# Kernel optimization log

Measured on AMD Instinct MI355X. Metric: run time of the kernel, lower is better.

The kernel has to match this reference:

```python
import jax, jax.numpy as jnp
import numpy as np

N = 100000   # nodes
E = 1600000  # edges
D = 64       # in_features == out_features (residual requires equality)
BN_EPS = 1e-5


def setup_inputs() -> dict:
    key = jax.random.key(0)
    ks = jax.random.split(key, 12)
    s = 1.0 / np.sqrt(D)
    inp = {
        "x": jax.random.normal(ks[0], (N, D), dtype=jnp.float32),
        "edge_index": jax.random.randint(ks[1], (2, E), 0, N, dtype=jnp.int64),
        # ResGatedGraphConv params: key/query/value/skip linears
        "Wk": jax.random.uniform(ks[2], (D, D), jnp.float32, -s, s),
        "bk": jax.random.uniform(ks[3], (D,), jnp.float32, -s, s),
        "Wq": jax.random.uniform(ks[4], (D, D), jnp.float32, -s, s),
        "bq": jax.random.uniform(ks[5], (D,), jnp.float32, -s, s),
        "Wv": jax.random.uniform(ks[6], (D, D), jnp.float32, -s, s),
        "bv": jax.random.uniform(ks[7], (D,), jnp.float32, -s, s),
        "Ws": jax.random.uniform(ks[8], (D, D), jnp.float32, -s, s),
        "bs": jax.random.uniform(ks[9], (D,), jnp.float32, -s, s),
        # BatchNorm1d affine params
        "gamma": jnp.ones((D,), jnp.float32),
        "beta": jnp.zeros((D,), jnp.float32),
    }
    return inp


def reference(x, edge_index, Wk, bk, Wq, bq, Wv, bv, Ws, bs, gamma, beta):
    # PyG ResGatedGraphConv:
    #   out_i = W_s x_i + b_s + sum_{(j->i)} sigmoid(k_i + q_j) * v_j
    # where k = lin_key(x), q = lin_query(x), v = lin_value(x).
    src = edge_index[0]  # source nodes j
    dst = edge_index[1]  # target nodes i

    k = x @ Wk.T + bk  # [N, D]
    q = x @ Wq.T + bq  # [N, D]
    v = x @ Wv.T + bv  # [N, D]

    gate = jax.nn.sigmoid(k[dst] + q[src])        # [E, D]
    msg = gate * v[src]                            # [E, D]
    agg = jax.ops.segment_sum(msg, dst, num_segments=x.shape[0])  # [N, D]

    h = agg + x @ Ws.T + bs

    # BatchNorm1d (training mode: batch statistics, biased variance)
    mean = jnp.mean(h, axis=0)
    var = jnp.var(h, axis=0)
    h = (h - mean) * jax.lax.rsqrt(var + BN_EPS) * gamma + beta

    h = jax.nn.relu(h)
    h = h + x  # residual
    # dropout: identity in eval / deterministic reference
    return h
```

## Files before the change

### kernel.cpp

```cpp
#include <hip/hip_runtime.h>
#include <hip/hip_bf16.h>
#include <math.h>

#define N_NODES 100000
#define N_EDGES 1600000
#define D_FEAT  64
#define BN_EPS  1e-5f

#define NBUCKET_PAD 256
#define BUCKET_SHIFT 9
#define NBLK_E  196
#define EPB     8192
#define HIST_TOTAL (NBUCKET_PAD * NBLK_E)
#define NCHUNK_H 98
#define DCAP    14336

typedef __attribute__((ext_vector_type(8))) short bf16x8;
typedef __attribute__((ext_vector_type(4))) float f32x4;

static __device__ __forceinline__ short f2bf(float f) {
    __hip_bfloat16 h = __float2bfloat16(f);
    return __builtin_bit_cast(short, h);
}


__global__ __launch_bounds__(256) void gemm4_mfma_kernel(
    const float* __restrict__ x,
    const float* __restrict__ Wk, const float* __restrict__ bk,
    const float* __restrict__ Wq, const float* __restrict__ bq,
    const float* __restrict__ Wv, const float* __restrict__ bv,
    const float* __restrict__ Ws, const float* __restrict__ bs,
    unsigned short* __restrict__ qvp,
    unsigned short* __restrict__ kp,
    float* __restrict__ h0)
{
    __shared__ short xs[64 * 64];

    const int lane = threadIdx.x & 63;
    const int wave = threadIdx.x >> 6;
    const int r0 = blockIdx.x * 64;

    const float* W; const float* b;
    if      (wave == 0) { W = Wk; b = bk; }
    else if (wave == 1) { W = Wq; b = bq; }
    else if (wave == 2) { W = Wv; b = bv; }
    else                { W = Ws; b = bs; }

    const int bcol = lane & 15;
    const int bk0  = (lane >> 4) * 8;
    bf16x8 bfrag[4][2];
    #pragma unroll
    for (int nt = 0; nt < 4; ++nt) {
        #pragma unroll
        for (int ks = 0; ks < 2; ++ks) {
            const float* wp = W + (nt * 16 + bcol) * 64 + ks * 32 + bk0;
            const float4 w0 = *reinterpret_cast<const float4*>(wp);
            const float4 w1 = *reinterpret_cast<const float4*>(wp + 4);
            bf16x8 f;
            f[0] = f2bf(w0.x); f[1] = f2bf(w0.y); f[2] = f2bf(w0.z); f[3] = f2bf(w0.w);
            f[4] = f2bf(w1.x); f[5] = f2bf(w1.y); f[6] = f2bf(w1.z); f[7] = f2bf(w1.w);
            bfrag[nt][ks] = f;
        }
    }
    float biasv[4];
    #pragma unroll
    for (int nt = 0; nt < 4; ++nt) biasv[nt] = b[nt * 16 + bcol];

    {
        const int row = threadIdx.x >> 2;
        const int qd  = threadIdx.x & 3;
        const int grow = r0 + row;
        float4 t0, t1, t2, t3;
        if (grow < N_NODES) {
            const float* xp = x + (size_t)grow * 64 + qd * 16;
            t0 = reinterpret_cast<const float4*>(xp)[0];
            t1 = reinterpret_cast<const float4*>(xp)[1];
            t2 = reinterpret_cast<const float4*>(xp)[2];
            t3 = reinterpret_cast<const float4*>(xp)[3];
        } else {
            t0 = t1 = t2 = t3 = make_float4(0.f, 0.f, 0.f, 0.f);
        }
        bf16x8 u0, u1;
        u0[0] = f2bf(t0.x); u0[1] = f2bf(t0.y); u0[2] = f2bf(t0.z); u0[3] = f2bf(t0.w);
        u0[4] = f2bf(t1.x); u0[5] = f2bf(t1.y); u0[6] = f2bf(t1.z); u0[7] = f2bf(t1.w);
        u1[0] = f2bf(t2.x); u1[1] = f2bf(t2.y); u1[2] = f2bf(t2.z); u1[3] = f2bf(t2.w);
        u1[4] = f2bf(t3.x); u1[5] = f2bf(t3.y); u1[6] = f2bf(t3.z); u1[7] = f2bf(t3.w);
        const int sw = row & 7;
        *reinterpret_cast<bf16x8*>(xs + row * 64 + (((qd * 2)     ^ sw) * 8)) = u0;
        *reinterpret_cast<bf16x8*>(xs + row * 64 + (((qd * 2 + 1) ^ sw) * 8)) = u1;
    }
    __syncthreads();

    f32x4 acc[4][4];
    #pragma unroll
    for (int mt = 0; mt < 4; ++mt)
        #pragma unroll
        for (int nt = 0; nt < 4; ++nt)
            acc[mt][nt] = (f32x4){biasv[nt], biasv[nt], biasv[nt], biasv[nt]};

    const int arow = lane & 15;
    const int ak   = lane >> 4;
    #pragma unroll
    for (int mt = 0; mt < 4; ++mt) {
        const int row = mt * 16 + arow;
        const int sw = row & 7;
        const bf16x8 a0 = *reinterpret_cast<const bf16x8*>(xs + row * 64 + ((ak       ^ sw) * 8));
        const bf16x8 a1 = *reinterpret_cast<const bf16x8*>(xs + row * 64 + (((4 + ak) ^ sw) * 8));
        #pragma unroll
        for (int nt = 0; nt < 4; ++nt) {
            acc[mt][nt] = __builtin_amdgcn_mfma_f32_16x16x32_bf16(
                a0, bfrag[nt][0], acc[mt][nt], 0, 0, 0);
            acc[mt][nt] = __builtin_amdgcn_mfma_f32_16x16x32_bf16(
                a1, bfrag[nt][1], acc[mt][nt], 0, 0, 0);
        }
    }

    const int crow0 = (lane >> 4) * 4;
    const int ccol  = lane & 15;
    #pragma unroll
    for (int mt = 0; mt < 4; ++mt) {
        #pragma unroll
        for (int nt = 0; nt < 4; ++nt) {
            #pragma unroll
            for (int r = 0; r < 4; ++r) {
                const int grow = r0 + mt * 16 + crow0 + r;
                if (grow < N_NODES) {
                    const int col = nt * 16 + ccol;
                    const float val = acc[mt][nt][r];
                    const size_t idx = (size_t)grow * 64 + col;
                    if      (wave == 0) kp[idx] = (unsigned short)f2bf(val);
                    else if (wave == 1) qvp[idx * 2]     = (unsigned short)f2bf(val);
                    else if (wave == 2) qvp[idx * 2 + 1] = (unsigned short)f2bf(val);
                    else                h0[idx] = val;
                }
            }
        }
    }
}

__global__ __launch_bounds__(256) void bucket_count_kernel(
    const int* __restrict__ ei, int* __restrict__ blockhist)
{
    __shared__ int h[NBUCKET_PAD];
    h[threadIdx.x] = 0;
    __syncthreads();
    const int base = blockIdx.x * EPB;
    for (int i = threadIdx.x; i < EPB; i += 256) {
        const int e = base + i;
        if (e < N_EDGES) atomicAdd(&h[ei[N_EDGES + e] >> BUCKET_SHIFT], 1);
    }
    __syncthreads();
    blockhist[threadIdx.x * NBLK_E + blockIdx.x] = h[threadIdx.x];
}

__global__ __launch_bounds__(256) void scan1_kernel(
    int* __restrict__ buf, int* __restrict__ chunk_sums, int total)
{
    __shared__ int sh[256];
    const int t = threadIdx.x;
    const int base = blockIdx.x * 512;
    const int i0 = base + 2 * t, i1 = base + 2 * t + 1;
    const int a = (i0 < total) ? buf[i0] : 0;
    const int b = (i1 < total) ? buf[i1] : 0;
    const int s = a + b;
    sh[t] = s;
    __syncthreads();
    for (int off = 1; off < 256; off <<= 1) {
        const int val = (t >= off) ? sh[t - off] : 0;
        __syncthreads();
        sh[t] += val;
        __syncthreads();
    }
    const int excl = sh[t] - s;
    if (i0 < total) buf[i0] = excl;
    if (i1 < total) buf[i1] = excl + a;
    if (t == 255) chunk_sums[blockIdx.x] = sh[255];
}

__global__ __launch_bounds__(256) void scan2_kernel(
    const int* __restrict__ chunk_sums, int* __restrict__ chunk_off, int nchunk)
{
    __shared__ int sh[256];
    const int t = threadIdx.x;
    const int v = (t < nchunk) ? chunk_sums[t] : 0;
    sh[t] = v;
    __syncthreads();
    for (int off = 1; off < 256; off <<= 1) {
        const int val = (t >= off) ? sh[t - off] : 0;
        __syncthreads();
        sh[t] += val;
        __syncthreads();
    }
    if (t < nchunk) chunk_off[t] = sh[t] - v;
}

__global__ __launch_bounds__(256) void scan3_kernel(
    int* __restrict__ buf, const int* __restrict__ chunk_off, int total)
{
    const int off = chunk_off[blockIdx.x];
    const int base = blockIdx.x * 512;
    #pragma unroll
    for (int k = 0; k < 2; ++k) {
        const int i = base + k * 256 + threadIdx.x;
        if (i < total) buf[i] += off;
    }
}

__global__ __launch_bounds__(256) void bucket_scatter_kernel(
    const int* __restrict__ ei, const int* __restrict__ blockhist,
    unsigned int* __restrict__ tmp)
{
    __shared__ int cur[NBUCKET_PAD];
    cur[threadIdx.x] = blockhist[threadIdx.x * NBLK_E + blockIdx.x];
    __syncthreads();
    const int base = blockIdx.x * EPB;
    for (int i = threadIdx.x; i < EPB; i += 256) {
        const int e = base + i;
        if (e < N_EDGES) {
            const int s = ei[e];
            const int d = ei[N_EDGES + e];
            const int pos = atomicAdd(&cur[d >> BUCKET_SHIFT], 1);
            tmp[pos] = ((unsigned int)s << BUCKET_SHIFT) | (unsigned int)(d & 511);
        }
    }
}

__global__ __launch_bounds__(512) void bucket_sort_kernel(
    const int* __restrict__ blockhist,
    unsigned int* __restrict__ tmp,
    int* __restrict__ row_start)
{
    __shared__ unsigned int stage[DCAP];
    __shared__ int hist[512];
    __shared__ int cursor[512];
    const int b = blockIdx.x;
    const int t = threadIdx.x;
    const int bstart = blockhist[b * NBLK_E];
    const int bend   = blockhist[(b + 1) * NBLK_E];
    int sz = bend - bstart;
    if (sz > DCAP) sz = DCAP;
    for (int i = t; i < sz; i += 512) stage[i] = tmp[bstart + i];
    hist[t] = 0;
    __syncthreads();
    for (int i = t; i < sz; i += 512) atomicAdd(&hist[stage[i] & 511], 1);
    __syncthreads();
    const int myv = hist[t];
    for (int off = 1; off < 512; off <<= 1) {
        const int u = (t >= off) ? hist[t - off] : 0;
        __syncthreads();
        hist[t] += u;
        __syncthreads();
    }
    const int excl = hist[t] - myv;
    const int node = b * 512 + t;
    if (node <= N_NODES) row_start[node] = bstart + excl;
    cursor[t] = excl;
    __syncthreads();
    for (int i = t; i < sz; i += 512) {
        const unsigned int pk = stage[i];
        const int pos = atomicAdd(&cursor[(int)(pk & 511)], 1);
        tmp[bstart + pos] = pk >> BUCKET_SHIFT;
    }
}

static __device__ __forceinline__ float edge_acc(float acc, float kf, unsigned int u) {
    const float qf = __uint_as_float(u << 16);
    const float vf = __uint_as_float(u & 0xffff0000u);
    const float s  = kf + qf;
    const float e  = __expf(-s);
    const float g  = __builtin_amdgcn_rcpf(1.0f + e);
    return fmaf(g, vf, acc);
}

__global__ __launch_bounds__(256) void gather_kernel(
    const unsigned int* __restrict__ qv,
    const unsigned short* __restrict__ kp,
    const int* __restrict__ row_start,
    const int* __restrict__ sorted_src,
    float* __restrict__ h0, float* __restrict__ stats)
{
    const int lane = threadIdx.x & 63;
    const int wave = threadIdx.x >> 6;
    float lsum = 0.0f, lsq = 0.0f;

    const int wid = blockIdx.x * 4 + wave;
    const int wstride = gridDim.x * 4;
    for (int n = wid; n < N_NODES; n += wstride) {
        const unsigned int kb = kp[(size_t)n * 64 + lane];
        const float kf = __uint_as_float(kb << 16);
        float acc = h0[(size_t)n * 64 + lane];
        const int base = row_start[n];
        const int end  = row_start[n + 1];
        int t = base;
        for (; t + 4 <= end; t += 4) {
            const int s0 = __builtin_amdgcn_readfirstlane(sorted_src[t + 0]);
            const int s1 = __builtin_amdgcn_readfirstlane(sorted_src[t + 1]);
            const int s2 = __builtin_amdgcn_readfirstlane(sorted_src[t + 2]);
            const int s3 = __builtin_amdgcn_readfirstlane(sorted_src[t + 3]);
            const unsigned int u0 = qv[(size_t)s0 * 64 + lane];
            const unsigned int u1 = qv[(size_t)s1 * 64 + lane];
            const unsigned int u2 = qv[(size_t)s2 * 64 + lane];
            const unsigned int u3 = qv[(size_t)s3 * 64 + lane];
            acc = edge_acc(acc, kf, u0);
            acc = edge_acc(acc, kf, u1);
            acc = edge_acc(acc, kf, u2);
            acc = edge_acc(acc, kf, u3);
        }
        for (; t < end; ++t) {
            const int s0 = __builtin_amdgcn_readfirstlane(sorted_src[t]);
            acc = edge_acc(acc, kf, qv[(size_t)s0 * 64 + lane]);
        }
        h0[(size_t)n * 64 + lane] = acc;
        lsum += acc;
        lsq  += acc * acc;
    }

    __shared__ float ls[4][64];
    __shared__ float lq[4][64];
    ls[wave][lane] = lsum;
    lq[wave][lane] = lsq;
    __syncthreads();
    if (threadIdx.x < 64) {
        const float ts = ls[0][lane] + ls[1][lane] + ls[2][lane] + ls[3][lane];
        const float tq = lq[0][lane] + lq[1][lane] + lq[2][lane] + lq[3][lane];
        atomicAdd(&stats[lane], ts);
        atomicAdd(&stats[64 + lane], tq);
    }
}

__global__ __launch_bounds__(256) void final_kernel(
    float* __restrict__ h0, const float* __restrict__ x,
    const float* __restrict__ stats,
    const float* __restrict__ gamma, const float* __restrict__ beta)
{
    const float invN = 1.0f / (float)N_NODES;
    const long long total = (long long)N_NODES * D_FEAT;
    for (long long idx = (long long)blockIdx.x * 256 + threadIdx.x;
         idx < total; idx += (long long)gridDim.x * 256) {
        const int i = (int)(idx & 63);
        const float mean = stats[i] * invN;
        const float var  = stats[64 + i] * invN - mean * mean;
        const float rstd = rsqrtf(var + BN_EPS);
        float y = (h0[idx] - mean) * rstd * gamma[i] + beta[i];
        y = fmaxf(y, 0.0f) + x[idx];
        h0[idx] = y;
    }
}

extern "C" void kernel_launch(void* const* d_in, const int* in_sizes, int n_in,
                              void* d_out, int out_size, void* d_ws, size_t ws_size,
                              hipStream_t stream)
{
    const float* x     = (const float*)d_in[0];
    const int*   ei    = (const int*)d_in[1];
    const float* Wk    = (const float*)d_in[2];
    const float* bk    = (const float*)d_in[3];
    const float* Wq    = (const float*)d_in[4];
    const float* bq    = (const float*)d_in[5];
    const float* Wv    = (const float*)d_in[6];
    const float* bv    = (const float*)d_in[7];
    const float* Ws    = (const float*)d_in[8];
    const float* bs    = (const float*)d_in[9];
    const float* gamma = (const float*)d_in[10];
    const float* beta  = (const float*)d_in[11];

    char* w = (char*)d_ws;
    unsigned int*   qv   = (unsigned int*)w;
    unsigned short* kpl  = (unsigned short*)(w + 25600000);
    float* stats      = (float*)(w + 38400000);
    int*   blockhist  = (int*)  (w + 38400512);
    int*   chunk_sums = (int*)  (w + 38601216);
    int*   chunk_off  = (int*)  (w + 38601608);
    int*   row_start  = (int*)  (w + 38602000);
    unsigned int* tmp = (unsigned int*)(w + 39002004);

    float* h0 = (float*)d_out;

    hipMemsetAsync(stats, 0, 128 * sizeof(float), stream);

    gemm4_mfma_kernel<<<(N_NODES + 63) / 64, 256, 0, stream>>>(
        x, Wk, bk, Wq, bq, Wv, bv, Ws, bs, (unsigned short*)qv, kpl, h0);

    bucket_count_kernel<<<NBLK_E, 256, 0, stream>>>(ei, blockhist);
    scan1_kernel<<<NCHUNK_H, 256, 0, stream>>>(blockhist, chunk_sums, HIST_TOTAL);
    scan2_kernel<<<1, 256, 0, stream>>>(chunk_sums, chunk_off, NCHUNK_H);
    scan3_kernel<<<NCHUNK_H, 256, 0, stream>>>(blockhist, chunk_off, HIST_TOTAL);
    bucket_scatter_kernel<<<NBLK_E, 256, 0, stream>>>(ei, blockhist, tmp);
    bucket_sort_kernel<<<196, 512, 0, stream>>>(blockhist, tmp, row_start);

    gather_kernel<<<2048, 256, 0, stream>>>(qv, kpl, row_start, (const int*)tmp, h0, stats);

    final_kernel<<<2048, 256, 0, stream>>>(h0, x, stats, gamma, beta);
}
```

Measured before the change: 219.8 us.

## Process four nodes per wave with 16 lanes each and 128-bit gathers

The gather kernel now assigns four destination nodes to each wave, with 16 lanes per node and each lane handling four features. Neighbour rows are fetched with uint4 loads, and edges past a node's degree are masked using a wave-wide max degree. The goal is fewer, wider memory requests and more independent loads in flight per wave. In exchange, lanes sit idle whenever degrees differ across the four nodes. Block statistics are now reduced with shared-memory atomics, and the launch bounds and grid size are adjusted.

Measured after the change: 219.0 us. No clear change (-0.4%).

```diff
diff --git a/kernel.cpp b/kernel.cpp
--- a/kernel.cpp
+++ b/kernel.cpp
@@ -263,16 +263,13 @@
     }
 }
 
-static __device__ __forceinline__ float edge_acc(float acc, float kf, unsigned int u) {
-    const float qf = __uint_as_float(u << 16);
-    const float vf = __uint_as_float(u & 0xffff0000u);
-    const float s  = kf + qf;
-    const float e  = __expf(-s);
-    const float g  = __builtin_amdgcn_rcpf(1.0f + e);
-    return fmaf(g, vf, acc);
-}
-
-__global__ __launch_bounds__(256) void gather_kernel(
+#define EDGE_F(u, kfj, accj) {                                        \
+    const float qf_ = __uint_as_float((u) << 16);                     \
+    const float vf_ = __uint_as_float((u) & 0xffff0000u);             \
+    const float e_  = __expf(-((kfj) + qf_));                         \
+    (accj) = fmaf(__builtin_amdgcn_rcpf(1.0f + e_), vf_, (accj)); }
+
+__global__ __launch_bounds__(256, 4) void gather_kernel(
     const unsigned int* __restrict__ qv,
     const unsigned short* __restrict__ kp,
     const int* __restrict__ row_start,
@@ -280,51 +277,84 @@
     float* __restrict__ h0, float* __restrict__ stats)
 {
     const int lane = threadIdx.x & 63;
+    const int sub  = lane >> 4;
+    const int l    = lane & 15;
     const int wave = threadIdx.x >> 6;
-    float lsum = 0.0f, lsq = 0.0f;
-
-    const int wid = blockIdx.x * 4 + wave;
-    const int wstride = gridDim.x * 4;
-    for (int n = wid; n < N_NODES; n += wstride) {
-        const unsigned int kb = kp[(size_t)n * 64 + lane];
-        const float kf = __uint_as_float(kb << 16);
-        float acc = h0[(size_t)n * 64 + lane];
+
+    float4 lsum = make_float4(0.f, 0.f, 0.f, 0.f);
+    float4 lsq  = make_float4(0.f, 0.f, 0.f, 0.f);
+
+    const int quad0  = blockIdx.x * 4 + wave;
+    const int qstride = gridDim.x * 4;
+    const int nquads = N_NODES / 4;
+
+    for (int quad = quad0; quad < nquads; quad += qstride) {
+        const int n = quad * 4 + sub;
         const int base = row_start[n];
         const int end  = row_start[n + 1];
-        int t = base;
-        for (; t + 4 <= end; t += 4) {
-            const int s0 = __builtin_amdgcn_readfirstlane(sorted_src[t + 0]);
-            const int s1 = __builtin_amdgcn_readfirstlane(sorted_src[t + 1]);
-            const int s2 = __builtin_amdgcn_readfirstlane(sorted_src[t + 2]);
-            const int s3 = __builtin_amdgcn_readfirstlane(sorted_src[t + 3]);
-            const unsigned int u0 = qv[(size_t)s0 * 64 + lane];
-            const unsigned int u1 = qv[(size_t)s1 * 64 + lane];
-            const unsigned int u2 = qv[(size_t)s2 * 64 + lane];
-            const unsigned int u3 = qv[(size_t)s3 * 64 + lane];
-            acc = edge_acc(acc, kf, u0);
-            acc = edge_acc(acc, kf, u1);
-            acc = edge_acc(acc, kf, u2);
-            acc = edge_acc(acc, kf, u3);
-        }
-        for (; t < end; ++t) {
-            const int s0 = __builtin_amdgcn_readfirstlane(sorted_src[t]);
-            acc = edge_acc(acc, kf, qv[(size_t)s0 * 64 + lane]);
-        }
-        h0[(size_t)n * 64 + lane] = acc;
-        lsum += acc;
-        lsq  += acc * acc;
-    }
-
-    __shared__ float ls[4][64];
-    __shared__ float lq[4][64];
-    ls[wave][lane] = lsum;
-    lq[wave][lane] = lsq;
+        const int deg  = end - base;
+
+        int m1 = max(deg, __shfl_xor(deg, 16));
+        const int maxdeg = max(m1, __shfl_xor(m1, 32));
+
+        const ushort4 kr = *reinterpret_cast<const ushort4*>(kp + (size_t)n * 64 + 4 * l);
+        float4 kf;
+        kf.x = __uint_as_float((unsigned int)kr.x << 16);
+        kf.y = __uint_as_float((unsigned int)kr.y << 16);
+        kf.z = __uint_as_float((unsigned int)kr.z << 16);
+        kf.w = __uint_as_float((unsigned int)kr.w << 16);
+        float4 acc = *reinterpret_cast<const float4*>(h0 + (size_t)n * 64 + 4 * l);
+
+        const int safe_last = max(min(end - 1, N_EDGES - 1), 0);
+
+        for (int t = 0; t < maxdeg; t += 4) {
+            const int i0 = min(base + t + 0, safe_last);
+            const int i1 = min(base + t + 1, safe_last);
+            const int i2 = min(base + t + 2, safe_last);
+            const int i3 = min(base + t + 3, safe_last);
+            const int s0 = sorted_src[i0];
+            const int s1 = sorted_src[i1];
+            const int s2 = sorted_src[i2];
+            const int s3 = sorted_src[i3];
+            uint4 U0 = *reinterpret_cast<const uint4*>(qv + (size_t)s0 * 64 + 4 * l);
+            uint4 U1 = *reinterpret_cast<const uint4*>(qv + (size_t)s1 * 64 + 4 * l);
+            uint4 U2 = *reinterpret_cast<const uint4*>(qv + (size_t)s2 * 64 + 4 * l);
+            uint4 U3 = *reinterpret_cast<const uint4*>(qv + (size_t)s3 * 64 + 4 * l);
+            const bool v0 = (t + 0) < deg, v1 = (t + 1) < deg,
+                       v2 = (t + 2) < deg, v3 = (t + 3) < deg;
+            U0.x = v0 ? U0.x : 0u; U0.y = v0 ? U0.y : 0u; U0.z = v0 ? U0.z : 0u; U0.w = v0 ? U0.w : 0u;
+            U1.x = v1 ? U1.x : 0u; U1.y = v1 ? U1.y : 0u; U1.z = v1 ? U1.z : 0u; U1.w = v1 ? U1.w : 0u;
+            U2.x = v2 ? U2.x : 0u; U2.y = v2 ? U2.y : 0u; U2.z = v2 ? U2.z : 0u; U2.w = v2 ? U2.w : 0u;
+            U3.x = v3 ? U3.x : 0u; U3.y = v3 ? U3.y : 0u; U3.z = v3 ? U3.z : 0u; U3.w = v3 ? U3.w : 0u;
+
+            EDGE_F(U0.x, kf.x, acc.x) EDGE_F(U0.y, kf.y, acc.y)
+            EDGE_F(U0.z, kf.z, acc.z) EDGE_F(U0.w, kf.w, acc.w)
+            EDGE_F(U1.x, kf.x, acc.x) EDGE_F(U1.y, kf.y, acc.y)
+            EDGE_F(U1.z, kf.z, acc.z) EDGE_F(U1.w, kf.w, acc.w)
+            EDGE_F(U2.x, kf.x, acc.x) EDGE_F(U2.y, kf.y, acc.y)
+            EDGE_F(U2.z, kf.z, acc.z) EDGE_F(U2.w, kf.w, acc.w)
+            EDGE_F(U3.x, kf.x, acc.x) EDGE_F(U3.y, kf.y, acc.y)
+            EDGE_F(U3.z, kf.z, acc.z) EDGE_F(U3.w, kf.w, acc.w)
+        }
+
+        *reinterpret_cast<float4*>(h0 + (size_t)n * 64 + 4 * l) = acc;
+        lsum.x += acc.x; lsum.y += acc.y; lsum.z += acc.z; lsum.w += acc.w;
+        lsq.x += acc.x * acc.x; lsq.y += acc.y * acc.y;
+        lsq.z += acc.z * acc.z; lsq.w += acc.w * acc.w;
+    }
+
+    __shared__ float bsum[64];
+    __shared__ float bsq[64];
+    if (threadIdx.x < 64) { bsum[threadIdx.x] = 0.f; bsq[threadIdx.x] = 0.f; }
+    __syncthreads();
+    atomicAdd(&bsum[4 * l + 0], lsum.x); atomicAdd(&bsq[4 * l + 0], lsq.x);
+    atomicAdd(&bsum[4 * l + 1], lsum.y); atomicAdd(&bsq[4 * l + 1], lsq.y);
+    atomicAdd(&bsum[4 * l + 2], lsum.z); atomicAdd(&bsq[4 * l + 2], lsq.z);
+    atomicAdd(&bsum[4 * l + 3], lsum.w); atomicAdd(&bsq[4 * l + 3], lsq.w);
     __syncthreads();
     if (threadIdx.x < 64) {
-        const float ts = ls[0][lane] + ls[1][lane] + ls[2][lane] + ls[3][lane];
-        const float tq = lq[0][lane] + lq[1][lane] + lq[2][lane] + lq[3][lane];
-        atomicAdd(&stats[lane], ts);
-        atomicAdd(&stats[64 + lane], tq);
+        atomicAdd(&stats[threadIdx.x], bsum[threadIdx.x]);
+        atomicAdd(&stats[64 + threadIdx.x], bsq[threadIdx.x]);
     }
 }
 
@@ -388,7 +418,7 @@
     bucket_scatter_kernel<<<NBLK_E, 256, 0, stream>>>(ei, blockhist, tmp);
     bucket_sort_kernel<<<196, 512, 0, stream>>>(blockhist, tmp, row_start);
 
-    gather_kernel<<<2048, 256, 0, stream>>>(qv, kpl, row_start, (const int*)tmp, h0, stats);
+    gather_kernel<<<2084, 256, 0, stream>>>(qv, kpl, row_start, (const int*)tmp, h0, stats);
 
     final_kernel<<<2048, 256, 0, stream>>>(h0, x, stats, gamma, beta);
 }
```
